# Optimization experiments

Hardware: AMD Instinct MI355X
Metric: run time of the kernel (lower is better)

Reference implementation:

```python
import jax, jax.numpy as jnp
import numpy as np
from jax import lax
from jax.scipy.special import logsumexp

TRIGGER_SIZE = 34
NTAG = TRIGGER_SIZE + 2  # +START/STOP
START = TRIGGER_SIZE
STOP = TRIGGER_SIZE + 1


def setup_inputs() -> dict:
    key = jax.random.key(0)
    k1, k2, k3, k4, k5 = jax.random.split(key, 5)
    B, S, H = 64, 512, 768
    x_1 = jax.random.normal(k1, (B, S, H), dtype=jnp.float32)
    head_indexes = jax.random.randint(k2, (B, S), 0, S)
    triggers_y = jax.random.randint(k3, (B, S), 0, TRIGGER_SIZE)
    W = jax.random.normal(k4, (H, NTAG), dtype=jnp.float32) * (1.0 / np.sqrt(H))
    b = jnp.zeros((NTAG,), dtype=jnp.float32)
    transitions = jax.random.normal(k5, (NTAG, NTAG), dtype=jnp.float32) * 0.1
    return {"x_1": x_1, "head_indexes": head_indexes, "triggers_y": triggers_y,
            "W": W, "b": b, "transitions": transitions}


def crf_nll(emit, mask, tags, trans):
    # emit [B,S,T], mask [B,S] bool, tags [B,S], trans [T,T] (from->to)
    B, S, T = emit.shape
    maskf = mask.astype(emit.dtype)
    # --- partition (forward algorithm) ---
    alpha0 = emit[:, 0] + trans[START][None, :]  # [B,T]; pos 0 always valid

    def fstep(alpha, inp):
        e_t, m_t = inp  # [B,T], [B]
        new = logsumexp(alpha[:, :, None] + trans[None, :, :], axis=1) + e_t
        return jnp.where(m_t[:, None], new, alpha), None

    alpha, _ = lax.scan(fstep, alpha0,
                        (emit[:, 1:].transpose(1, 0, 2), mask[:, 1:].T))
    logZ = logsumexp(alpha + trans[:, STOP][None, :], axis=1)  # [B]
    # --- gold path score ---
    emit_g = jnp.take_along_axis(emit, tags[:, :, None], axis=2)[..., 0]  # [B,S]
    emit_score = (emit_g * maskf).sum(axis=1)
    trans_pair = trans[tags[:, :-1], tags[:, 1:]]  # [B,S-1]
    trans_score = (trans_pair * maskf[:, 1:]).sum(axis=1)
    xlen = mask.sum(axis=1)  # [B]
    last_tag = jnp.take_along_axis(tags, (xlen - 1)[:, None], axis=1)[:, 0]
    gold = emit_score + trans[START, tags[:, 0]] + trans_score + trans[last_tag, STOP]
    return jnp.sum(logZ - gold)


def crf_viterbi(emit, mask, trans):
    B, S, T = emit.shape
    ids = jnp.arange(T)
    delta0 = emit[:, 0] + trans[START][None, :]

    def vstep(delta, inp):
        e_t, m_t = inp
        scores = delta[:, :, None] + trans[None, :, :]  # [B,T,T]
        best = scores.max(axis=1) + e_t
        bp = jnp.argmax(scores, axis=1)  # [B,T]
        new_delta = jnp.where(m_t[:, None], best, delta)
        bp = jnp.where(m_t[:, None], bp, ids[None, :])  # identity on pad
        return new_delta, bp

    delta, bps = lax.scan(vstep, delta0,
                          (emit[:, 1:].transpose(1, 0, 2), mask[:, 1:].T))
    final = delta + trans[:, STOP][None, :]
    last_tag = jnp.argmax(final, axis=1)  # [B]
    path_score = jnp.max(final, axis=1)

    def back(tag_next, bp_t):
        tag_t = jnp.take_along_axis(bp_t, tag_next[:, None], axis=1)[:, 0]
        return tag_t, tag_t

    _, prev_tags = lax.scan(back, last_tag, bps, reverse=True)  # [S-1,B]
    path = jnp.concatenate([prev_tags.T, last_tag[:, None]], axis=1)  # [B,S]
    path = jnp.where(mask, path, 0)
    return path_score, path


def reference(x_1, head_indexes, triggers_y, W, b, transitions):
    B, S, H = x_1.shape
    # batched version of the per-sample index_select loop
    x = jnp.take_along_axis(x_1, head_indexes[:, :, None], axis=1)  # [B,S,H]
    xlen = head_indexes.max(axis=1)  # xlen = [max(row) for row in head_indexes]
    mask = jnp.arange(S)[None, :] < xlen[:, None]  # [B,S] bool
    logits = jax.nn.leaky_relu(x @ W + b)  # tri_fc1 + leaky_relu (dropout=eval)
    trigger_loss = crf_nll(logits, mask, triggers_y, transitions)
    path_score, trigger_hat = crf_viterbi(logits, mask, transitions)
    return trigger_loss, trigger_hat, path_score
```

## Files before the change

### kernel.cpp

```cpp
#include <hip/hip_runtime.h>
#include <math.h>

#define SB 64
#define SS 512
#define SH 768
#define NT 36
#define TSTART 34
#define TSTOP 35
#define NC 32
#define CL 16

#define CFENCE() asm volatile("" ::: "memory")

__device__ __forceinline__ float wave_max_f(float v) {
#pragma unroll
    for (int off = 32; off > 0; off >>= 1) v = fmaxf(v, __shfl_xor(v, off, 64));
    return v;
}
__device__ __forceinline__ float wave_sum_f(float v) {
#pragma unroll
    for (int off = 32; off > 0; off >>= 1) v += __shfl_xor(v, off, 64);
    return v;
}
__device__ __forceinline__ float bcast0(float v) {
    return __uint_as_float(__builtin_amdgcn_readfirstlane(__float_as_uint(v)));
}

#define XP 129
#define XBUF 8256
#define RED(qq, rr, jj) smem[(qq) * 2368 + (rr) * 37 + (jj)]

extern "C" __global__ __launch_bounds__(512) void k_emit(
    const float* __restrict__ x1, const int* __restrict__ hidx,
    const float* __restrict__ W, const float* __restrict__ bias,
    float* __restrict__ emit)
{
    __shared__ __align__(16) float smem[18944];

    int tid  = threadIdx.x;
    int lane = tid & 63;
    int q    = __builtin_amdgcn_readfirstlane(tid >> 6);

    int srow = tid >> 3;
    int c8   = tid & 7;
    int grs  = blockIdx.x * 64 + srow;
    int bs   = grs >> 9;
    const float4* srcRow = (const float4*)(x1 + (size_t)(bs * SS + hidx[grs]) * SH);
    int woff = srow * XP + c8 * 4;

    float acc[NT];
#pragma unroll
    for (int j = 0; j < NT; ++j) acc[j] = 0.f;

    float4 n0, n1, n2, n3;
    n0 = srcRow[c8];  n1 = srcRow[c8 + 8];
    n2 = srcRow[c8 + 16]; n3 = srcRow[c8 + 24];
    {
        float* d = smem + woff;
        d[0] = n0.x; d[1] = n0.y; d[2] = n0.z; d[3] = n0.w;
        d[32] = n1.x; d[33] = n1.y; d[34] = n1.z; d[35] = n1.w;
        d[64] = n2.x; d[65] = n2.y; d[66] = n2.z; d[67] = n2.w;
        d[96] = n3.x; d[97] = n3.y; d[98] = n3.z; d[99] = n3.w;
    }

#pragma unroll
    for (int s = 0; s < 6; ++s) {
        if (s < 5) {
            int f0 = (s + 1) * 32 + c8;
            n0 = srcRow[f0]; n1 = srcRow[f0 + 8];
            n2 = srcRow[f0 + 16]; n3 = srcRow[f0 + 24];
        }
        __syncthreads();
        {
            const float* xs = smem + (s & 1) * XBUF + lane * XP + 16 * q;
            const float* Ws = W + (size_t)(128 * s + 16 * q) * NT;
#pragma unroll
            for (int k = 0; k < 16; ++k) {
                float xv = xs[k];
                const float* wr = Ws + k * NT;
#pragma unroll
                for (int j = 0; j < NT; ++j) acc[j] += xv * wr[j];
            }
        }
        if (s < 5) {
            float* d = smem + ((s + 1) & 1) * XBUF + woff;
            d[0] = n0.x; d[1] = n0.y; d[2] = n0.z; d[3] = n0.w;
            d[32] = n1.x; d[33] = n1.y; d[34] = n1.z; d[35] = n1.w;
            d[64] = n2.x; d[65] = n2.y; d[66] = n2.z; d[67] = n2.w;
            d[96] = n3.x; d[97] = n3.y; d[98] = n3.z; d[99] = n3.w;
        }
    }
    __syncthreads();

#pragma unroll
    for (int j = 0; j < NT; ++j) RED(q, lane, j) = acc[j];
    __syncthreads();

    int r = tid >> 2, g = tid & 3;
    float vout[9];
    if (tid < 256) {
#pragma unroll
        for (int jj = 0; jj < 9; ++jj) {
            int j = g * 9 + jj;
            float v = bias[j];
#pragma unroll
            for (int qq = 0; qq < 8; ++qq) v += RED(qq, r, j);
            vout[jj] = v > 0.f ? v : 0.01f * v;
        }
    }
    __syncthreads();
    if (tid < 256) {
#pragma unroll
        for (int jj = 0; jj < 9; ++jj) smem[r * NT + g * 9 + jj] = vout[jj];
    }
    __syncthreads();
    {
        const float4* st4 = (const float4*)smem;
        float4* op = (float4*)(emit + (size_t)blockIdx.x * 64 * NT);
        for (int i = tid; i < 576; i += 512) op[i] = st4[i];
    }
}

#define STEP2(T, WRITEBP)                                                 \
    {                                                                     \
        float e_t = elsw[((T) - t0s) * NT + jj];                          \
        float mL = bcast0(aL);                                            \
        bcL[lane] = __expf(aL - mL);                                      \
        bcV[lane] = aV;                                                   \
        CFENCE();                                                         \
        __builtin_amdgcn_wave_barrier();                                  \
        float s0 = 0.f, s1 = 0.f, s2 = 0.f, s3 = 0.f;                     \
        float b0 = -1e30f, b1 = -1e30f, b2 = -1e30f, b3 = -1e30f;         \
        int   i0 = 0, i1 = 1, i2 = 2, i3 = 3;                             \
        _Pragma("unroll")                                                 \
        for (int k = 0; k < 9; ++k) {                                     \
            float4 pv = bcL4[w][k];                                       \
            float4 dv = bcV4[w][k];                                       \
            s0 += pv.x * Ecol[4 * k];                                     \
            s1 += pv.y * Ecol[4 * k + 1];                                 \
            s2 += pv.z * Ecol[4 * k + 2];                                 \
            s3 += pv.w * Ecol[4 * k + 3];                                 \
            float c0 = dv.x + tcol[4 * k];                                \
            float c1 = dv.y + tcol[4 * k + 1];                            \
            float c2 = dv.z + tcol[4 * k + 2];                            \
            float c3 = dv.w + tcol[4 * k + 3];                            \
            if (c0 > b0) { b0 = c0; i0 = 4 * k; }                         \
            if (c1 > b1) { b1 = c1; i1 = 4 * k + 1; }                     \
            if (c2 > b2) { b2 = c2; i2 = 4 * k + 2; }                     \
            if (c3 > b3) { b3 = c3; i3 = 4 * k + 3; }                     \
        }                                                                 \
        CFENCE();                                                         \
        float anewL = mL + __logf((s0 + s1) + (s2 + s3)) + e_t;           \
        float best = b0; int bi = i0;                                     \
        if (b1 > best || (b1 == best && i1 < bi)) { best = b1; bi = i1; } \
        if (b2 > best || (b2 == best && i2 < bi)) { best = b2; bi = i2; } \
        if (b3 > best || (b3 == best && i3 < bi)) { best = b3; bi = i3; } \
        aL = act ? anewL : -1e30f;                                        \
        aV = act ? (best + e_t) : -1e30f;                                 \
        if ((WRITEBP) && act)                                             \
            bp[((size_t)b * SS + (T)) * 64 + jj] = (unsigned char)bi;     \
    }

extern "C" __global__ __launch_bounds__(256) void k_scan(
    const float* __restrict__ emit, const int* __restrict__ hidx,
    const float* __restrict__ trans,
    float* __restrict__ Warr, float* __restrict__ Earr,
    float* __restrict__ lse_local,
    float* __restrict__ score_local, int* __restrict__ ltag,
    unsigned char* __restrict__ bp)
{
    __shared__ float trl[NT * NT];
    __shared__ float els[4][1024];
    __shared__ float4 bcL4[4][16];
    __shared__ float4 bcV4[4][16];

    int tid  = threadIdx.x;
    int lane = tid & 63;
    int w    = __builtin_amdgcn_readfirstlane(tid >> 6);

    int wid  = blockIdx.x * 4 + w;
    int b    = wid >> 5;
    int c    = wid & 31;

    const float* eb  = emit + (size_t)b * SS * NT;
    int t0s = (c > 0) ? (c * CL - 9) : 0;
    const float* ebase = eb + (size_t)t0s * NT;
    float* elsw = els[w];

#pragma unroll
    for (int i = 0; i < 4; ++i) {
        __builtin_amdgcn_global_load_lds(
            (const __attribute__((address_space(1))) void*)(ebase + i * 256 + lane * 4),
            (__attribute__((address_space(3))) void*)(elsw + i * 256), 16, 0, 0);
    }
    for (int i = tid; i < NT * NT; i += 256) trl[i] = trans[i];

    int  jj  = lane < NT ? lane : NT - 1;
    bool act = lane < NT;

    int xm = 0;
    const int* hb = hidx + b * SS;
#pragma unroll
    for (int k = 0; k < SS / 64; ++k) xm = max(xm, hb[lane + 64 * k]);
#pragma unroll
    for (int off = 32; off > 0; off >>= 1) xm = max(xm, __shfl_xor(xm, off, 64));
    int xlen = xm;
    int cl   = (xlen >= 1) ? ((xlen - 1) >> 4) : 0;

    int tb0 = c * CL - 8;
    int te0 = c * CL; if (te0 > xlen) te0 = xlen; te0 -= 1;
    int tb  = c * CL; if (tb < 1) tb = 1;
    int te  = (c + 1) * CL; if (te > xlen) te = xlen; te -= 1;

    float init;
    if (c == 0) init = act ? (eb[jj] + trans[TSTART * NT + jj]) : -1e30f;
    else        init = act ? eb[(size_t)(tb0 - 1) * NT + jj] : -1e30f;
    float aL = init, aV = init;

    __syncthreads();

    float* bcL = (float*)bcL4[w];
    float* bcV = (float*)bcV4[w];

    float tcol[NT], Ecol[NT];
#pragma unroll
    for (int i = 0; i < NT; ++i) {
        tcol[i] = trl[i * NT + jj];
        Ecol[i] = __expf(tcol[i]);
    }

    if (c > 0) {
        for (int t = tb0; t <= te0; ++t) STEP2(t, 0)
    }
    float WvL = bcast0(aL), WvV = bcast0(aV);
    for (int t = tb; t <= te; ++t) STEP2(t, 1)
    float EvL = bcast0(aL), EvV = bcast0(aV);

    if (lane == 0) {
        Warr[b * NC + c]        = WvL;
        Earr[b * NC + c]        = EvL;
        Warr[(SB + b) * NC + c] = WvV;
        Earr[(SB + b) * NC + c] = EvV;
    }

    if (c == cl) {
        float ffL = act ? (aL + trl[jj * NT + TSTOP]) : -1e30f;
        float M = wave_max_f(ffL);
        float ssum = wave_sum_f(__expf(ffL - M));
        if (lane == 0) lse_local[b] = M + __logf(ssum);

        float ffV = act ? (aV + trl[jj * NT + TSTOP]) : -1e30f;
        float bv = ffV; int bi = lane;
#pragma unroll
        for (int off = 32; off > 0; off >>= 1) {
            float ov = __shfl_xor(bv, off, 64);
            int   oi = __shfl_xor(bi, off, 64);
            if (ov > bv || (ov == bv && oi < bi)) { bv = ov; bi = oi; }
        }
        if (lane == 0) { score_local[b] = bv; ltag[b] = bi; }
    }
}

extern "C" __global__ __launch_bounds__(1024) void k_final(
    const float* __restrict__ emit, const int* __restrict__ hidx,
    const int* __restrict__ tags, const float* __restrict__ trans,
    const float* __restrict__ Warr, const float* __restrict__ Earr,
    const float* __restrict__ lse_local,
    const float* __restrict__ score_local, const int* __restrict__ ltag,
    const unsigned char* __restrict__ bp,
    float* __restrict__ loss_out, float* __restrict__ path_out,
    float* __restrict__ score_out)
{
    __shared__ unsigned char bpl[SS * 64];
    __shared__ unsigned char cmap[SS][40];
    __shared__ unsigned char exitmap[NC][64];
    __shared__ float gred[16];
    __shared__ int   ent[NC];

    int tid  = threadIdx.x;
    int lane = tid & 63;
    int w    = tid >> 6;
    int b    = blockIdx.x;

    {
        const int4* src = (const int4*)(bp + (size_t)b * SS * 64);
        int4* dst = (int4*)bpl;
        for (int i = tid; i < SS * 4; i += 1024) dst[i] = src[i];
    }

    int xm = 0;
    const int* hb = hidx + b * SS;
#pragma unroll
    for (int k = 0; k < SS / 64; ++k) xm = max(xm, hb[lane + 64 * k]);
#pragma unroll
    for (int off = 32; off > 0; off >>= 1) xm = max(xm, __shfl_xor(xm, off, 64));
    int xlen = xm;
    int cl   = (xlen >= 1) ? ((xlen - 1) >> 4) : 0;

    float g = 0.f;
    const int* tg = tags + b * SS;
    if (tid < SS) {
        int t = tid;
        if (t < xlen) {
            int tt = tg[t];
            g += emit[((size_t)b * SS + t) * NT + tt];
            if (t >= 1) g += trans[tg[t - 1] * NT + tt];
        }
    }
    g = wave_sum_f(g);
    if (lane == 0) gred[w] = g;

    float kf = 0.f, kv = 0.f;
    if (w == 8) {
        if (lane < cl) {
            kf = Earr[(0 * SB + b) * NC + lane] - Warr[(0 * SB + b) * NC + lane + 1];
            kv = Earr[(1 * SB + b) * NC + lane] - Warr[(1 * SB + b) * NC + lane + 1];
        }
        kf = wave_sum_f(kf);
        kv = wave_sum_f(kv);
    }

    __syncthreads();

    if (tid == 512) {
        float gold = 0.f;
#pragma unroll
        for (int i = 0; i < 8; ++i) gold += gred[i];
        int tg0 = tg[0];
        int lt  = (xlen >= 1) ? tg[xlen - 1] : tg0;
        gold += trans[TSTART * NT + tg0] + trans[lt * NT + TSTOP];
        atomicAdd(loss_out, (lse_local[b] + kf) - gold);
        score_out[b] = score_local[b] + kv;
    }

    for (int cc = 0; cc < 2; ++cc) {
        int c = w * 2 + cc;
        if (xlen >= 1 && c <= cl) {
            int tb = (c == 0) ? 1 : c * CL;
            int te = c * CL + CL - 1; if (te > xlen - 1) te = xlen - 1;
            int m = lane;
            if (lane < NT) cmap[te][lane] = (unsigned char)m;
            for (int t = te; t >= tb; --t) {
                m = bpl[t * 64 + m];
                if (lane < NT) {
                    if (t > tb || c == 0) cmap[t - 1][lane] = (unsigned char)m;
                    else                  exitmap[c][lane]  = (unsigned char)m;
                }
            }
        }
    }
    __syncthreads();

    if (tid == 0 && xlen >= 1) {
        int e = ltag[b];
        for (int c2 = cl; c2 >= 0; --c2) {
            ent[c2] = e;
            if (c2 > 0) e = exitmap[c2][e];
        }
    }
    __syncthreads();

    if (tid < SS) {
        int t = tid;
        float* op = path_out + (size_t)b * SS;
        if (t >= xlen) op[t] = 0.f;
        else           op[t] = (float)cmap[t][ent[t >> 4]];
    }
}

extern "C" void kernel_launch(void* const* d_in, const int* in_sizes, int n_in,
                              void* d_out, int out_size, void* d_ws, size_t ws_size,
                              hipStream_t stream)
{
    const float* x1    = (const float*)d_in[0];
    const int*   hidx  = (const int*)d_in[1];
    const int*   tags  = (const int*)d_in[2];
    const float* W     = (const float*)d_in[3];
    const float* bias  = (const float*)d_in[4];
    const float* trans = (const float*)d_in[5];
    float* out = (float*)d_out;

    float* emit        = (float*)d_ws;
    float* Warr        = emit + (size_t)SB * SS * NT;
    float* Earr        = Warr + 2 * SB * NC;
    float* lse_local   = Earr + 2 * SB * NC;
    float* score_local = lse_local + SB;
    int*   ltag        = (int*)(score_local + SB);
    float* spacer      = (float*)(ltag + SB);
    unsigned char* bp  = (unsigned char*)(spacer + SB);

    hipLaunchKernelGGL(k_emit, dim3(SB * SS / 64), dim3(512), 0, stream,
                       x1, hidx, W, bias, emit);
    hipLaunchKernelGGL(k_scan, dim3(512), dim3(256), 0, stream,
                       emit, hidx, trans, Warr, Earr, lse_local,
                       score_local, ltag, bp);
    hipLaunchKernelGGL(k_final, dim3(SB), dim3(1024), 0, stream,
                       emit, hidx, tags, trans, Warr, Earr, lse_local,
                       score_local, ltag, bp, out, out + 1, out + 1 + SB * SS);
}
```

Measured before the change: 222.2 us.

## Split GEMV K dimension across two blocks and fuse bias/activation into consumers

The emission kernel now launches twice as many blocks, each handling half of the hidden dimension, and writes two partial sums (emitA, emitB) with a tree reduction across waves in place of a full 8-way shared reduction. Shared memory per block is halved so more blocks can be resident. Bias add and leaky ReLU move into the scan and final kernels, which now read and combine both partial buffers. This adds extra global traffic for the second partial buffer and replaces the async global-to-LDS load in the scan kernel with a plain load-and-compute loop.

After: 260.0 us. 1.17x slower.

```diff
diff --git a/kernel.cpp b/kernel.cpp
--- a/kernel.cpp
+++ b/kernel.cpp
@@ -26,56 +26,53 @@
     return __uint_as_float(__builtin_amdgcn_readfirstlane(__float_as_uint(v)));
 }
 
-#define XP 129
-#define XBUF 8256
-#define RED(qq, rr, jj) smem[(qq) * 2368 + (rr) * 37 + (jj)]
-
-extern "C" __global__ __launch_bounds__(512) void k_emit(
+#define XP 65
+#define XBUFF 4160
+#define RED(p, r, j) smem[(p) * 2368 + (r) * 37 + (j)]
+
+extern "C" __global__ __launch_bounds__(512, 8) void k_emit(
     const float* __restrict__ x1, const int* __restrict__ hidx,
     const float* __restrict__ W, const float* __restrict__ bias,
-    float* __restrict__ emit)
+    float* __restrict__ emitA, float* __restrict__ emitB)
 {
-    __shared__ __align__(16) float smem[18944];
+    __shared__ __align__(16) float smem[9472];
 
     int tid  = threadIdx.x;
     int lane = tid & 63;
     int q    = __builtin_amdgcn_readfirstlane(tid >> 6);
+    int kb   = blockIdx.x & 1;
+    int rb   = blockIdx.x >> 1;
 
     int srow = tid >> 3;
     int c8   = tid & 7;
-    int grs  = blockIdx.x * 64 + srow;
+    int grs  = rb * 64 + srow;
     int bs   = grs >> 9;
-    const float4* srcRow = (const float4*)(x1 + (size_t)(bs * SS + hidx[grs]) * SH);
-    int woff = srow * XP + c8 * 4;
+    const float4* srcRow = (const float4*)(x1 + (size_t)(bs * SS + hidx[grs]) * SH) + kb * 96;
+    int woff = srow * XP + c8 * 8;
 
     float acc[NT];
 #pragma unroll
     for (int j = 0; j < NT; ++j) acc[j] = 0.f;
 
-    float4 n0, n1, n2, n3;
-    n0 = srcRow[c8];  n1 = srcRow[c8 + 8];
-    n2 = srcRow[c8 + 16]; n3 = srcRow[c8 + 24];
+    float4 n0 = srcRow[2 * c8], n1 = srcRow[2 * c8 + 1];
     {
         float* d = smem + woff;
         d[0] = n0.x; d[1] = n0.y; d[2] = n0.z; d[3] = n0.w;
-        d[32] = n1.x; d[33] = n1.y; d[34] = n1.z; d[35] = n1.w;
-        d[64] = n2.x; d[65] = n2.y; d[66] = n2.z; d[67] = n2.w;
-        d[96] = n3.x; d[97] = n3.y; d[98] = n3.z; d[99] = n3.w;
+        d[4] = n1.x; d[5] = n1.y; d[6] = n1.z; d[7] = n1.w;
     }
 
 #pragma unroll
     for (int s = 0; s < 6; ++s) {
         if (s < 5) {
-            int f0 = (s + 1) * 32 + c8;
-            n0 = srcRow[f0]; n1 = srcRow[f0 + 8];
-            n2 = srcRow[f0 + 16]; n3 = srcRow[f0 + 24];
+            int f0 = (s + 1) * 16 + 2 * c8;
+            n0 = srcRow[f0]; n1 = srcRow[f0 + 1];
         }
         __syncthreads();
         {
-            const float* xs = smem + (s & 1) * XBUF + lane * XP + 16 * q;
-            const float* Ws = W + (size_t)(128 * s + 16 * q) * NT;
-#pragma unroll
-            for (int k = 0; k < 16; ++k) {
+            const float* xs = smem + (s & 1) * XBUFF + lane * XP + 8 * q;
+            const float* Ws = W + (size_t)(kb * 384 + 64 * s + 8 * q) * NT;
+#pragma unroll
+            for (int k = 0; k < 8; ++k) {
                 float xv = xs[k];
                 const float* wr = Ws + k * NT;
 #pragma unroll
@@ -83,41 +80,47 @@
             }
         }
         if (s < 5) {
-            float* d = smem + ((s + 1) & 1) * XBUF + woff;
+            float* d = smem + ((s + 1) & 1) * XBUFF + woff;
             d[0] = n0.x; d[1] = n0.y; d[2] = n0.z; d[3] = n0.w;
-            d[32] = n1.x; d[33] = n1.y; d[34] = n1.z; d[35] = n1.w;
-            d[64] = n2.x; d[65] = n2.y; d[66] = n2.z; d[67] = n2.w;
-            d[96] = n3.x; d[97] = n3.y; d[98] = n3.z; d[99] = n3.w;
-        }
-    }
-    __syncthreads();
-
-#pragma unroll
-    for (int j = 0; j < NT; ++j) RED(q, lane, j) = acc[j];
-    __syncthreads();
-
-    int r = tid >> 2, g = tid & 3;
-    float vout[9];
-    if (tid < 256) {
-#pragma unroll
-        for (int jj = 0; jj < 9; ++jj) {
-            int j = g * 9 + jj;
-            float v = bias[j];
-#pragma unroll
-            for (int qq = 0; qq < 8; ++qq) v += RED(qq, r, j);
-            vout[jj] = v > 0.f ? v : 0.01f * v;
-        }
-    }
-    __syncthreads();
-    if (tid < 256) {
-#pragma unroll
-        for (int jj = 0; jj < 9; ++jj) smem[r * NT + g * 9 + jj] = vout[jj];
-    }
-    __syncthreads();
-    {
-        const float4* st4 = (const float4*)smem;
-        float4* op = (float4*)(emit + (size_t)blockIdx.x * 64 * NT);
-        for (int i = tid; i < 576; i += 512) op[i] = st4[i];
+            d[4] = n1.x; d[5] = n1.y; d[6] = n1.z; d[7] = n1.w;
+        }
+    }
+    __syncthreads();
+
+    if (q >= 4) {
+#pragma unroll
+        for (int j = 0; j < NT; ++j) RED(q - 4, lane, j) = acc[j];
+    }
+    __syncthreads();
+    if (q < 4) {
+#pragma unroll
+        for (int j = 0; j < NT; ++j) acc[j] += RED(q, lane, j);
+    }
+    __syncthreads();
+    if (q == 2 || q == 3) {
+#pragma unroll
+        for (int j = 0; j < NT; ++j) RED(q - 2, lane, j) = acc[j];
+    }
+    __syncthreads();
+    if (q < 2) {
+#pragma unroll
+        for (int j = 0; j < NT; ++j) acc[j] += RED(q, lane, j);
+    }
+    __syncthreads();
+    if (q == 1) {
+#pragma unroll
+        for (int j = 0; j < NT; ++j) RED(1, lane, j) = acc[j];
+    }
+    __syncthreads();
+    if (q == 0) {
+        alignas(16) float vout[NT];
+#pragma unroll
+        for (int j = 0; j < NT; ++j) vout[j] = acc[j] + RED(1, lane, j);
+        float* outp = kb ? emitB : emitA;
+        float4* op = (float4*)(outp + (size_t)(rb * 64 + lane) * NT);
+        const float4* vv = (const float4*)vout;
+#pragma unroll
+        for (int i = 0; i < 9; ++i) op[i] = vv[i];
     }
 }
 
@@ -162,15 +165,17 @@
     }
 
 extern "C" __global__ __launch_bounds__(256) void k_scan(
-    const float* __restrict__ emit, const int* __restrict__ hidx,
-    const float* __restrict__ trans,
+    const float* __restrict__ emA, const float* __restrict__ emB,
+    const float* __restrict__ bias,
+    const int* __restrict__ hidx, const float* __restrict__ trans,
     float* __restrict__ Warr, float* __restrict__ Earr,
     float* __restrict__ lse_local,
     float* __restrict__ score_local, int* __restrict__ ltag,
     unsigned char* __restrict__ bp)
 {
     __shared__ float trl[NT * NT];
-    __shared__ float els[4][1024];
+    __shared__ float bbl[40];
+    __shared__ __align__(16) float els[4][1024];
     __shared__ float4 bcL4[4][16];
     __shared__ float4 bcV4[4][16];
 
@@ -182,18 +187,13 @@
     int b    = wid >> 5;
     int c    = wid & 31;
 
-    const float* eb  = emit + (size_t)b * SS * NT;
+    size_t eboff = (size_t)b * SS * NT;
     int t0s = (c > 0) ? (c * CL - 9) : 0;
-    const float* ebase = eb + (size_t)t0s * NT;
+    size_t wbase = eboff + (size_t)t0s * NT;
     float* elsw = els[w];
 
-#pragma unroll
-    for (int i = 0; i < 4; ++i) {
-        __builtin_amdgcn_global_load_lds(
-            (const __attribute__((address_space(1))) void*)(ebase + i * 256 + lane * 4),
-            (__attribute__((address_space(3))) void*)(elsw + i * 256), 16, 0, 0);
-    }
     for (int i = tid; i < NT * NT; i += 256) trl[i] = trans[i];
+    if (tid < NT) bbl[tid] = bias[tid];
 
     int  jj  = lane < NT ? lane : NT - 1;
     bool act = lane < NT;
@@ -212,12 +212,40 @@
     int tb  = c * CL; if (tb < 1) tb = 1;
     int te  = (c + 1) * CL; if (te > xlen) te = xlen; te -= 1;
 
+    __syncthreads();
+
+    {
+        const float4* A4 = (const float4*)(emA + wbase);
+        const float4* B4 = (const float4*)(emB + wbase);
+        float4* E4 = (float4*)elsw;
+        for (int i4 = lane; i4 < 256; i4 += 64) {
+            float4 a = A4[i4], bb = B4[i4];
+            int f0 = i4 * 4;
+            int j0 = f0 % 36;
+            int j1 = (j0 + 1 == 36) ? 0 : j0 + 1;
+            int j2 = (j1 + 1 == 36) ? 0 : j1 + 1;
+            int j3 = (j2 + 1 == 36) ? 0 : j2 + 1;
+            float4 v;
+            v.x = a.x + bb.x + bbl[j0]; v.x = v.x > 0.f ? v.x : 0.01f * v.x;
+            v.y = a.y + bb.y + bbl[j1]; v.y = v.y > 0.f ? v.y : 0.01f * v.y;
+            v.z = a.z + bb.z + bbl[j2]; v.z = v.z > 0.f ? v.z : 0.01f * v.z;
+            v.w = a.w + bb.w + bbl[j3]; v.w = v.w > 0.f ? v.w : 0.01f * v.w;
+            E4[i4] = v;
+        }
+    }
+
     float init;
-    if (c == 0) init = act ? (eb[jj] + trans[TSTART * NT + jj]) : -1e30f;
-    else        init = act ? eb[(size_t)(tb0 - 1) * NT + jj] : -1e30f;
+    if (c == 0) {
+        float ev = emA[eboff + jj] + emB[eboff + jj] + bbl[jj];
+        ev = ev > 0.f ? ev : 0.01f * ev;
+        init = act ? (ev + trl[TSTART * NT + jj]) : -1e30f;
+    } else {
+        size_t gi = eboff + (size_t)(tb0 - 1) * NT + jj;
+        float ev = emA[gi] + emB[gi] + bbl[jj];
+        ev = ev > 0.f ? ev : 0.01f * ev;
+        init = act ? ev : -1e30f;
+    }
     float aL = init, aV = init;
-
-    __syncthreads();
 
     float* bcL = (float*)bcL4[w];
     float* bcV = (float*)bcV4[w];
@@ -262,7 +290,9 @@
 }
 
 extern "C" __global__ __launch_bounds__(1024) void k_final(
-    const float* __restrict__ emit, const int* __restrict__ hidx,
+    const float* __restrict__ emA, const float* __restrict__ emB,
+    const float* __restrict__ bias,
+    const int* __restrict__ hidx,
     const int* __restrict__ tags, const float* __restrict__ trans,
     const float* __restrict__ Warr, const float* __restrict__ Earr,
     const float* __restrict__ lse_local,
@@ -303,7 +333,10 @@
         int t = tid;
         if (t < xlen) {
             int tt = tg[t];
-            g += emit[((size_t)b * SS + t) * NT + tt];
+            size_t gi = ((size_t)b * SS + t) * NT + tt;
+            float ev = emA[gi] + emB[gi] + bias[tt];
+            ev = ev > 0.f ? ev : 0.01f * ev;
+            g += ev;
             if (t >= 1) g += trans[tg[t - 1] * NT + tt];
         }
     }
@@ -380,8 +413,9 @@
     const float* trans = (const float*)d_in[5];
     float* out = (float*)d_out;
 
-    float* emit        = (float*)d_ws;
-    float* Warr        = emit + (size_t)SB * SS * NT;
+    float* emitA       = (float*)d_ws;
+    float* emitB       = emitA + (size_t)SB * SS * NT;
+    float* Warr        = emitB + (size_t)SB * SS * NT;
     float* Earr        = Warr + 2 * SB * NC;
     float* lse_local   = Earr + 2 * SB * NC;
     float* score_local = lse_local + SB;
@@ -389,12 +423,13 @@
     float* spacer      = (float*)(ltag + SB);
     unsigned char* bp  = (unsigned char*)(spacer + SB);
 
-    hipLaunchKernelGGL(k_emit, dim3(SB * SS / 64), dim3(512), 0, stream,
-                       x1, hidx, W, bias, emit);
+    hipLaunchKernelGGL(k_emit, dim3(SB * SS / 64 * 2), dim3(512), 0, stream,
+                       x1, hidx, W, bias, emitA, emitB);
     hipLaunchKernelGGL(k_scan, dim3(512), dim3(256), 0, stream,
-                       emit, hidx, trans, Warr, Earr, lse_local,
+                       emitA, emitB, bias, hidx, trans, Warr, Earr, lse_local,
                        score_local, ltag, bp);
     hipLaunchKernelGGL(k_final, dim3(SB), dim3(1024), 0, stream,
-                       emit, hidx, tags, trans, Warr, Earr, lse_local,
-                       score_local, ltag, bp, out, out + 1, out + 1 + SB * SS);
-}
+                       emitA, emitB, bias, hidx, tags, trans, Warr, Earr,
+                       lse_local, score_local, ltag, bp,
+                       out, out + 1, out + 1 + SB * SS);
+}
```
